# Optimization experiments

Hardware: AMD Instinct MI355X
Metric: run time of the kernel (lower is better)

## Reference

```python
import jax, jax.numpy as jnp
import numpy as np

B, S, D = 2, 2048, 1024
H, DK = 16, 64            # num_heads, d_kv; inner_dim = H*DK = 1024
NUM_BUCKETS = 32
MAX_DISTANCE = 128


def _relative_position_bucket(relative_position, bidirectional=True,
                              num_buckets=NUM_BUCKETS, max_distance=MAX_DISTANCE):
    # Faithful port of Mesh-TF / HF T5 bucketing (int32 in, int32 buckets out).
    relative_buckets = jnp.zeros_like(relative_position)
    if bidirectional:
        num_buckets = num_buckets // 2
        relative_buckets = relative_buckets + (relative_position > 0).astype(jnp.int32) * num_buckets
        relative_position = jnp.abs(relative_position)
    else:
        relative_position = -jnp.minimum(relative_position, 0)
    max_exact = num_buckets // 2
    is_small = relative_position < max_exact
    # log-spaced buckets for large distances; guard log(0) (masked by is_small anyway)
    rel_f = jnp.maximum(relative_position, 1).astype(jnp.float32)
    val_if_large = max_exact + (
        jnp.log(rel_f / max_exact) / np.log(max_distance / max_exact) * (num_buckets - max_exact)
    ).astype(jnp.int32)
    val_if_large = jnp.minimum(val_if_large, num_buckets - 1)
    return relative_buckets + jnp.where(is_small, relative_position, val_if_large)


def compute_bias(rel_emb, query_length, key_length):
    ctx = jnp.arange(query_length, dtype=jnp.int32)[:, None]
    mem = jnp.arange(key_length, dtype=jnp.int32)[None, :]
    buckets = _relative_position_bucket(mem - ctx, bidirectional=True)  # [q, k]
    values = rel_emb[buckets]                       # [q, k, H]
    return jnp.transpose(values, (2, 0, 1))[None]   # [1, H, q, k]


def setup_inputs() -> dict:
    key = jax.random.key(0)
    ks = jax.random.split(key, 6)
    scale = 1.0 / np.sqrt(D)
    return {
        "hidden_states": jax.random.normal(ks[0], (B, S, D), jnp.float32),
        "wq": jax.random.normal(ks[1], (D, H * DK), jnp.float32) * scale,
        "wk": jax.random.normal(ks[2], (D, H * DK), jnp.float32) * scale,
        "wv": jax.random.normal(ks[3], (D, H * DK), jnp.float32) * scale,
        "wo": jax.random.normal(ks[4], (H * DK, D), jnp.float32) * scale,
        "rel_emb": jax.random.normal(ks[5], (NUM_BUCKETS, H), jnp.float32),
    }


def reference(hidden_states, wq, wk, wv, wo, rel_emb):
    b, s, _ = hidden_states.shape

    def shape(x):  # [B,S,H*DK] -> [B,H,S,DK]
        return x.reshape(b, s, H, DK).transpose(0, 2, 1, 3)

    q = shape(hidden_states @ wq)   # NOTE: T5 does not scale q by 1/sqrt(d_kv)
    k = shape(hidden_states @ wk)
    v = shape(hidden_states @ wv)

    scores = jnp.einsum("bhqd,bhkd->bhqk", q, k)
    position_bias = compute_bias(rel_emb, s, s)     # [1,H,S,S]
    scores = scores + position_bias
    attn = jax.nn.softmax(scores, axis=-1)
    ctx = jnp.einsum("bhqk,bhkd->bhqd", attn, v)    # [B,H,S,DK]
    ctx = ctx.transpose(0, 2, 1, 3).reshape(b, s, H * DK)
    return ctx @ wo
```

## Files before the change

kernel.cpp:

```cpp
#include <hip/hip_runtime.h>


typedef __attribute__((ext_vector_type(8)))  unsigned short u16x8;
typedef __attribute__((ext_vector_type(4)))  unsigned short u16x4;
typedef __attribute__((ext_vector_type(8)))  __bf16         bf16x8;
typedef __attribute__((ext_vector_type(4)))  float          f32x4;
typedef __attribute__((ext_vector_type(4)))  unsigned int   u32x4;

#define GLOBAL_AS __attribute__((address_space(1)))
#define LDS_AS    __attribute__((address_space(3)))

static __device__ inline f32x4 MFMA(u16x8 a, u16x8 b, f32x4 c) {
  return __builtin_amdgcn_mfma_f32_16x16x32_bf16(
      __builtin_bit_cast(bf16x8, a), __builtin_bit_cast(bf16x8, b), c, 0, 0, 0);
}

static __device__ inline void gload16(const void* g, void* l) {
  __builtin_amdgcn_global_load_lds((const GLOBAL_AS unsigned int*)g,
                                   (LDS_AS unsigned int*)l, 16, 0, 0);
}

static __device__ inline unsigned short f2bf(float x) {
  unsigned int u = __builtin_bit_cast(unsigned int, x);
  u = (u + 0x7FFFu + ((u >> 16) & 1u)) >> 16;
  return (unsigned short)u;
}

static __device__ inline unsigned int cvtpk(float lo, float hi) {
  unsigned int r;
  asm volatile("v_cvt_pk_bf16_f32 %0, %1, %2" : "=v"(r) : "v"(lo), "v"(hi));
  return r;
}

#define L2E 1.4426950408889634f

__global__ void k_cvt(const float* __restrict__ src, unsigned short* __restrict__ dst, int n4) {
  int i = blockIdx.x * blockDim.x + threadIdx.x;
  if (i >= n4) return;
  float4 v = *(const float4*)(src + (size_t)i * 4);
  u16x4 o;
  o[0] = f2bf(v.x); o[1] = f2bf(v.y); o[2] = f2bf(v.z); o[3] = f2bf(v.w);
  *(u16x4*)(dst + (size_t)i * 4) = o;
}

__global__ __launch_bounds__(256) void k_tc(const float* __restrict__ src,
                                            unsigned short* __restrict__ dst,
                                            int K, int N) {
  __shared__ float tile[64][65];
  int k0 = blockIdx.y << 6, n0 = blockIdx.x << 6;
  int t = threadIdx.x;
  int rr = t >> 4, cc = (t & 15) << 2;
#pragma unroll
  for (int j = 0; j < 4; j++) {
    float4 v = *(const float4*)(src + (size_t)(k0 + rr + j * 16) * N + n0 + cc);
    tile[rr + j * 16][cc + 0] = v.x;
    tile[rr + j * 16][cc + 1] = v.y;
    tile[rr + j * 16][cc + 2] = v.z;
    tile[rr + j * 16][cc + 3] = v.w;
  }
  __syncthreads();
#pragma unroll
  for (int j = 0; j < 4; j++) {
    int n = rr + j * 16;
    u16x4 o;
    o[0] = f2bf(tile[cc + 0][n]);
    o[1] = f2bf(tile[cc + 1][n]);
    o[2] = f2bf(tile[cc + 2][n]);
    o[3] = f2bf(tile[cc + 3][n]);
    *(u16x4*)(dst + (size_t)(n0 + n) * K + k0 + cc) = o;
  }
}

__global__ void k_bias(const float* __restrict__ rel_emb, float* __restrict__ btab) {
  int i = blockIdx.x * blockDim.x + threadIdx.x;
  if (i >= 16 * 4095) return;
  int h = i / 4095;
  int rp = i % 4095 - 2047;
  int rb = rp > 0 ? 16 : 0;
  int arp = rp < 0 ? -rp : rp;
  int v;
  if (arp < 8) {
    v = arp;
  } else {
    float t = logf((float)arp * 0.125f);
    t = t / 2.772588722239781f;
    t = t * 8.0f;
    v = 8 + (int)t;
    if (v > 15) v = 15;
  }
  btab[i] = rel_emb[(rb + v) * 16 + h] * L2E;
}

template <int EPI>
__global__ __launch_bounds__(256) void k_gemm(const unsigned short* __restrict__ A,
                                              const unsigned short* __restrict__ Bt,
                                              void* __restrict__ outp,
                                              int M, int N, int K) {
  __shared__ __attribute__((aligned(16))) char smem[32768];
  const int tid = threadIdx.x;
  const int lane = tid & 63, w = tid >> 6;
  const int l15 = lane & 15, g = lane >> 4;
  const int wr = w >> 1, wc = w & 1;
  const int bm0 = blockIdx.y << 7, bn0 = blockIdx.x << 7;

  const char* Ag = (const char*)A + (size_t)bm0 * K * 2;
  const char* Bg = (const char*)Bt + (size_t)bn0 * K * 2;

  f32x4 acc[4][4];
#pragma unroll
  for (int i = 0; i < 4; i++)
#pragma unroll
    for (int j = 0; j < 4; j++) acc[i][j] = (f32x4)0.0f;

  const int rowA = wr * 64 + l15;
  const int rowB = wc * 64 + l15;
  const int swz = (l15 & 7) << 4;

  for (int kt = 0; kt < K; kt += 64) {
#pragma unroll
    for (int j = 0; j < 4; j++) {
      int idx = ((j * 4 + w) << 10) + (lane << 4);
      int row = idx >> 7;
      int gs = (idx >> 4) & 7;
      size_t co = (size_t)row * (K * 2) + kt * 2 + ((gs ^ (row & 7)) << 4);
      gload16(Ag + co, smem + ((j * 4 + w) << 10));
      gload16(Bg + co, smem + 16384 + ((j * 4 + w) << 10));
    }
    __syncthreads();
#pragma unroll
    for (int kk = 0; kk < 2; kk++) {
      const int cp = ((kk << 6) + (g << 4)) ^ swz;
      u16x8 af[4], bfv[4];
#pragma unroll
      for (int mt = 0; mt < 4; mt++)
        af[mt] = *(const u16x8*)(smem + ((rowA + mt * 16) << 7) + cp);
#pragma unroll
      for (int nt = 0; nt < 4; nt++)
        bfv[nt] = *(const u16x8*)(smem + 16384 + ((rowB + nt * 16) << 7) + cp);
#pragma unroll
      for (int mt = 0; mt < 4; mt++)
#pragma unroll
        for (int nt = 0; nt < 4; nt++)
          acc[mt][nt] = MFMA(af[mt], bfv[nt], acc[mt][nt]);
    }
    __syncthreads();
  }

#pragma unroll
  for (int mt = 0; mt < 4; mt++) {
#pragma unroll
    for (int nt = 0; nt < 4; nt++) {
#pragma unroll
      for (int r = 0; r < 4; r++) {
        int m = bm0 + wr * 64 + mt * 16 + g * 4 + r;
        int n = bn0 + wc * 64 + nt * 16 + l15;
        float val = acc[mt][nt][r];
        if (EPI == 0) {
          int which = n >> 10;
          int hh = (n >> 6) & 15;
          int d = n & 63;
          int bb = m >> 11, s = m & 2047;
          int plane = bb * 16 + hh;
          unsigned short* o = (unsigned short*)outp;
          if (which == 0) {
            o[(size_t)plane * 131072 + (size_t)s * 64 + d] = f2bf(val * L2E);
          } else if (which == 1) {
            o[4194304 + (size_t)plane * 131072 + (size_t)s * 64 + d] = f2bf(val);
          } else {
            o[8388608 + (size_t)plane * 131072 + (size_t)d * 2048 + s] = f2bf(val);
          }
        } else {
          ((float*)outp)[(size_t)m * N + n] = val;
        }
      }
    }
  }
}

__global__ __launch_bounds__(512, 6) void k_attn(const unsigned short* __restrict__ qkv,
                                                 const float* __restrict__ btab,
                                                 unsigned short* __restrict__ ctx) {
  __shared__ __attribute__((aligned(16))) char smem[32768];
  const int tid = threadIdx.x;
  const int lane = tid & 63, w = tid >> 6;
  const int l15 = lane & 15, g = lane >> 4;

  const int wg = ((blockIdx.x & 7) << 6) + (blockIdx.x >> 3);
  const int plane = wg >> 4, qb = wg & 15;
  const int h = plane & 15, b = plane >> 4;
  const int q0 = (qb << 7) + (w << 4);

  const unsigned short* Qp = qkv + (size_t)plane * 131072;
  const unsigned short* Kp = qkv + 4194304 + (size_t)plane * 131072;
  const unsigned short* Vt = qkv + 8388608 + (size_t)plane * 131072;

  u16x8 qa[2];
#pragma unroll
  for (int kk = 0; kk < 2; kk++)
    qa[kk] = *(const u16x8*)(Qp + (size_t)(q0 + l15) * 64 + kk * 32 + g * 8);

  float m_r = -1e30f;
  f32x4 oacc[4], lacc;
#pragma unroll
  for (int t = 0; t < 4; t++) oacc[t] = (f32x4)0.0f;
  lacc = (f32x4)0.0f;

  const float* brow = btab + h * 4095 + 2047 - q0;
  const float cpos = btab[h * 4095 + 2047 + 1024];
  const float cneg = btab[h * 4095 + 2047 - 1024];

  u16x8 ones;
  {
    u32x4 ov = {0x3F803F80u, 0x3F803F80u, 0x3F803F80u, 0x3F803F80u};
    ones = __builtin_bit_cast(u16x8, ov);
  }

  const int srow = (w << 3) + (lane >> 3);
  const int soff = ((lane & 7) ^ (srow & 7)) << 4;
  const char* Ksrc = (const char*)Kp + (size_t)srow * 128 + soff;
  const char* Vsrc = (const char*)Vt + (size_t)srow * 4096 + soff;

  auto STAGE = [&](int t, int bsel) {
    char* sb = smem + (bsel << 14) + (w << 10);
    gload16(Ksrc + (size_t)t * 8192, sb);
    gload16(Vsrc + (size_t)t * 128, sb + 8192);
  };

  STAGE(0, 0);
  __syncthreads();

  for (int t = 0; t < 32; ++t) {
    const int c = t & 1;
    if (t < 31) STAGE(t + 1, c ^ 1);
    const char* kb = smem + (c << 14);
    const char* vbuf = kb + 8192;
    const int kv = t << 6;

    f32x4 s[4];
    __builtin_amdgcn_s_setprio(1);
#pragma unroll
    for (int nt = 0; nt < 4; nt++) {
      int keyr = nt * 16 + l15;
      int sw = (keyr & 7) << 4;
      u16x8 kb0 = *(const u16x8*)(kb + (keyr << 7) + ((g << 4) ^ sw));
      u16x8 kb1 = *(const u16x8*)(kb + (keyr << 7) + ((64 + (g << 4)) ^ sw));
      f32x4 z = (f32x4)0.0f;
      z = MFMA(kb0, qa[0], z);
      z = MFMA(kb1, qa[1], z);
      s[nt] = z;
    }
    __builtin_amdgcn_s_setprio(0);

    int delta = kv - q0;
    float cb;
    if (delta >= 112 || delta <= -160) {
      cb = delta > 0 ? cpos : cneg;
    } else {
      cb = 0.0f;
      const float* bp = brow + kv + (g << 2) - l15;
#pragma unroll
      for (int nt = 0; nt < 4; nt++)
#pragma unroll
        for (int r = 0; r < 4; r++) s[nt][r] += bp[nt * 16 + r];
    }

    float m1 = fmaxf(fmaxf(s[0][0], s[0][1]), s[0][2]);
    float m2 = fmaxf(fmaxf(s[0][3], s[1][0]), s[1][1]);
    float m3 = fmaxf(fmaxf(s[1][2], s[1][3]), s[2][0]);
    float m4 = fmaxf(fmaxf(s[2][1], s[2][2]), s[2][3]);
    float m5 = fmaxf(fmaxf(s[3][0], s[3][1]), s[3][2]);
    float mloc = fmaxf(fmaxf(fmaxf(m1, m2), fmaxf(m3, m4)), fmaxf(m5, s[3][3]));

    if (!__all(mloc + cb <= m_r + 12.0f)) {
      float mxrow = fmaxf(mloc, __shfl_xor(mloc, 16));
      mxrow = fmaxf(mxrow, __shfl_xor(mxrow, 32));
      float mnew = fmaxf(m_r, mxrow + cb);
      float alpha = exp2f(m_r - mnew);
      m_r = mnew;
      float a4[4];
#pragma unroll
      for (int r = 0; r < 4; r++) a4[r] = __shfl(alpha, (g << 2) + r);
#pragma unroll
      for (int tt = 0; tt < 4; tt++) {
        f32x4 o = oacc[tt];
        o[0] *= a4[0]; o[1] *= a4[1]; o[2] *= a4[2]; o[3] *= a4[3];
        oacc[tt] = o;
      }
      lacc[0] *= a4[0]; lacc[1] *= a4[1]; lacc[2] *= a4[2]; lacc[3] *= a4[3];
    }

    float eb = cb - m_r;
#pragma unroll
    for (int nt = 0; nt < 4; nt++)
#pragma unroll
      for (int r = 0; r < 4; r++)
        s[nt][r] = __builtin_amdgcn_exp2f(s[nt][r] + eb);

    unsigned int wpk[4][2];
#pragma unroll
    for (int nt = 0; nt < 4; nt++) {
      wpk[nt][0] = cvtpk(s[nt][0], s[nt][1]);
      wpk[nt][1] = cvtpk(s[nt][2], s[nt][3]);
    }
    u16x8 pa[2];
#pragma unroll
    for (int kk = 0; kk < 2; kk++) {
      unsigned int X0 = wpk[2 * kk][0], Y0 = wpk[2 * kk + 1][0];
      asm volatile("v_permlane32_swap_b32 %0, %1" : "+v"(X0), "+v"(Y0));
      asm volatile("v_permlane16_swap_b32 %0, %1" : "+v"(X0), "+v"(Y0));
      unsigned int X1 = wpk[2 * kk][1], Y1 = wpk[2 * kk + 1][1];
      asm volatile("v_permlane32_swap_b32 %0, %1" : "+v"(X1), "+v"(Y1));
      asm volatile("v_permlane16_swap_b32 %0, %1" : "+v"(X1), "+v"(Y1));
      u32x4 pw = {X0, X1, Y0, Y1};
      pa[kk] = __builtin_bit_cast(u16x8, pw);
    }

    __builtin_amdgcn_s_setprio(1);
#pragma unroll
    for (int tt = 0; tt < 4; tt++) {
      int d = tt * 16 + l15;
      int sw = (d & 7) << 4;
      u16x8 vb0 = *(const u16x8*)(vbuf + (d << 7) + ((g << 4) ^ sw));
      u16x8 vb1 = *(const u16x8*)(vbuf + (d << 7) + ((64 + (g << 4)) ^ sw));
      oacc[tt] = MFMA(pa[0], vb0, oacc[tt]);
      oacc[tt] = MFMA(pa[1], vb1, oacc[tt]);
    }
    lacc = MFMA(pa[0], ones, lacc);
    lacc = MFMA(pa[1], ones, lacc);
    __builtin_amdgcn_s_setprio(0);

    __syncthreads();
  }

#pragma unroll
  for (int r = 0; r < 4; r++) {
    float inv = 1.0f / lacc[r];
    size_t rowoff = ((size_t)(b * 2048 + q0 + (g << 2) + r) << 10) + h * 64;
#pragma unroll
    for (int tt = 0; tt < 4; tt++)
      ctx[rowoff + tt * 16 + l15] = f2bf(oacc[tt][r] * inv);
  }
}

extern "C" void kernel_launch(void* const* d_in, const int* in_sizes, int n_in,
                              void* d_out, int out_size, void* d_ws, size_t ws_size,
                              hipStream_t stream) {
  const float* hs = (const float*)d_in[0];
  const float* wq = (const float*)d_in[1];
  const float* wk = (const float*)d_in[2];
  const float* wv = (const float*)d_in[3];
  const float* wo = (const float*)d_in[4];
  const float* re = (const float*)d_in[5];

  if (ws_size < 50593728u) return;

  char* ws = (char*)d_ws;
  unsigned short* hsb = (unsigned short*)(ws);
  unsigned short* wt  = (unsigned short*)(ws + 8388608);
  unsigned short* wot = (unsigned short*)(ws + 14680064);
  unsigned short* qkv = (unsigned short*)(ws + 16777216);
  unsigned short* ctx = (unsigned short*)(ws + 41943040);
  float*          btab = (float*)(ws + 50331648);

  k_cvt<<<4096, 256, 0, stream>>>(hs, hsb, 1048576);
  k_tc<<<dim3(16, 16), 256, 0, stream>>>(wq, wt, 1024, 1024);
  k_tc<<<dim3(16, 16), 256, 0, stream>>>(wk, wt + 1048576, 1024, 1024);
  k_tc<<<dim3(16, 16), 256, 0, stream>>>(wv, wt + 2097152, 1024, 1024);
  k_tc<<<dim3(16, 16), 256, 0, stream>>>(wo, wot, 1024, 1024);
  k_bias<<<256, 256, 0, stream>>>(re, btab);

  k_gemm<0><<<dim3(24, 32), 256, 0, stream>>>(hsb, wt, qkv, 4096, 3072, 1024);
  k_attn<<<512, 512, 0, stream>>>(qkv, btab, ctx);
  k_gemm<1><<<dim3(8, 32), 256, 0, stream>>>(ctx, wot, d_out, 4096, 1024, 1024);
}
```

Baseline: 134.5 us.

## Fuse prep kernels into one launch and triple-buffer attention K/V staging

```diff
diff --git a/kernel.cpp b/kernel.cpp
--- a/kernel.cpp
+++ b/kernel.cpp
@@ -34,61 +34,76 @@
 
 #define L2E 1.4426950408889634f
 
-__global__ void k_cvt(const float* __restrict__ src, unsigned short* __restrict__ dst, int n4) {
-  int i = blockIdx.x * blockDim.x + threadIdx.x;
-  if (i >= n4) return;
-  float4 v = *(const float4*)(src + (size_t)i * 4);
-  u16x4 o;
-  o[0] = f2bf(v.x); o[1] = f2bf(v.y); o[2] = f2bf(v.z); o[3] = f2bf(v.w);
-  *(u16x4*)(dst + (size_t)i * 4) = o;
-}
-
-__global__ __launch_bounds__(256) void k_tc(const float* __restrict__ src,
-                                            unsigned short* __restrict__ dst,
-                                            int K, int N) {
+__global__ __launch_bounds__(256) void k_prep(const float* __restrict__ hs,
+                                              const float* __restrict__ wq,
+                                              const float* __restrict__ wk,
+                                              const float* __restrict__ wv,
+                                              const float* __restrict__ wo,
+                                              const float* __restrict__ re,
+                                              unsigned short* __restrict__ hsb,
+                                              unsigned short* __restrict__ wt,
+                                              unsigned short* __restrict__ wot,
+                                              float* __restrict__ btab) {
   __shared__ float tile[64][65];
-  int k0 = blockIdx.y << 6, n0 = blockIdx.x << 6;
-  int t = threadIdx.x;
-  int rr = t >> 4, cc = (t & 15) << 2;
-#pragma unroll
-  for (int j = 0; j < 4; j++) {
-    float4 v = *(const float4*)(src + (size_t)(k0 + rr + j * 16) * N + n0 + cc);
-    tile[rr + j * 16][cc + 0] = v.x;
-    tile[rr + j * 16][cc + 1] = v.y;
-    tile[rr + j * 16][cc + 2] = v.z;
-    tile[rr + j * 16][cc + 3] = v.w;
-  }
-  __syncthreads();
-#pragma unroll
-  for (int j = 0; j < 4; j++) {
-    int n = rr + j * 16;
+  const int bid = blockIdx.x;
+  const int t = threadIdx.x;
+
+  if (bid < 4096) {
+    int i = bid * 256 + t;
+    float4 v = *(const float4*)(hs + (size_t)i * 4);
     u16x4 o;
-    o[0] = f2bf(tile[cc + 0][n]);
-    o[1] = f2bf(tile[cc + 1][n]);
-    o[2] = f2bf(tile[cc + 2][n]);
-    o[3] = f2bf(tile[cc + 3][n]);
-    *(u16x4*)(dst + (size_t)(n0 + n) * K + k0 + cc) = o;
-  }
-}
-
-__global__ void k_bias(const float* __restrict__ rel_emb, float* __restrict__ btab) {
-  int i = blockIdx.x * blockDim.x + threadIdx.x;
-  if (i >= 16 * 4095) return;
-  int h = i / 4095;
-  int rp = i % 4095 - 2047;
-  int rb = rp > 0 ? 16 : 0;
-  int arp = rp < 0 ? -rp : rp;
-  int v;
-  if (arp < 8) {
-    v = arp;
+    o[0] = f2bf(v.x); o[1] = f2bf(v.y); o[2] = f2bf(v.z); o[3] = f2bf(v.w);
+    *(u16x4*)(hsb + (size_t)i * 4) = o;
+  } else if (bid < 5120) {
+    int sub = bid - 4096;
+    int which = sub >> 8;
+    int sb = sub & 255;
+    int n0 = (sb & 15) << 6, k0 = (sb >> 4) << 6;
+    const float* src = which == 0 ? wq : which == 1 ? wk : which == 2 ? wv : wo;
+    unsigned short* dst = which == 0 ? wt
+                        : which == 1 ? wt + 1048576
+                        : which == 2 ? wt + 2097152 : wot;
+    const int K = 1024, N = 1024;
+    int rr = t >> 4, cc = (t & 15) << 2;
+#pragma unroll
+    for (int j = 0; j < 4; j++) {
+      float4 v = *(const float4*)(src + (size_t)(k0 + rr + j * 16) * N + n0 + cc);
+      tile[rr + j * 16][cc + 0] = v.x;
+      tile[rr + j * 16][cc + 1] = v.y;
+      tile[rr + j * 16][cc + 2] = v.z;
+      tile[rr + j * 16][cc + 3] = v.w;
+    }
+    __syncthreads();
+#pragma unroll
+    for (int j = 0; j < 4; j++) {
+      int n = rr + j * 16;
+      u16x4 o;
+      o[0] = f2bf(tile[cc + 0][n]);
+      o[1] = f2bf(tile[cc + 1][n]);
+      o[2] = f2bf(tile[cc + 2][n]);
+      o[3] = f2bf(tile[cc + 3][n]);
+      *(u16x4*)(dst + (size_t)(n0 + n) * K + k0 + cc) = o;
+    }
   } else {
-    float t = logf((float)arp * 0.125f);
-    t = t / 2.772588722239781f;
-    t = t * 8.0f;
-    v = 8 + (int)t;
-    if (v > 15) v = 15;
-  }
-  btab[i] = rel_emb[(rb + v) * 16 + h] * L2E;
+    int i = (bid - 5120) * 256 + t;
+    if (i < 16 * 4095) {
+      int h = i / 4095;
+      int rp = i % 4095 - 2047;
+      int rb = rp > 0 ? 16 : 0;
+      int arp = rp < 0 ? -rp : rp;
+      int v;
+      if (arp < 8) {
+        v = arp;
+      } else {
+        float tt = logf((float)arp * 0.125f);
+        tt = tt / 2.772588722239781f;
+        tt = tt * 8.0f;
+        v = 8 + (int)tt;
+        if (v > 15) v = 15;
+      }
+      btab[i] = re[(rb + v) * 16 + h] * L2E;
+    }
+  }
 }
 
 template <int EPI>
@@ -180,7 +195,7 @@
 __global__ __launch_bounds__(512, 6) void k_attn(const unsigned short* __restrict__ qkv,
                                                  const float* __restrict__ btab,
                                                  unsigned short* __restrict__ ctx) {
-  __shared__ __attribute__((aligned(16))) char smem[32768];
+  __shared__ __attribute__((aligned(16))) char smem[49152];
   const int tid = threadIdx.x;
   const int lane = tid & 63, w = tid >> 6;
   const int l15 = lane & 15, g = lane >> 4;
@@ -221,19 +236,25 @@
   const char* Vsrc = (const char*)Vt + (size_t)srow * 4096 + soff;
 
   auto STAGE = [&](int t, int bsel) {
-    char* sb = smem + (bsel << 14) + (w << 10);
+    char* sb = smem + bsel * 16384 + (w << 10);
     gload16(Ksrc + (size_t)t * 8192, sb);
     gload16(Vsrc + (size_t)t * 128, sb + 8192);
   };
 
   STAGE(0, 0);
-  __syncthreads();
-
+  STAGE(1, 1);
+
+  int rb = 0, sbn = 2;
   for (int t = 0; t < 32; ++t) {
-    const int c = t & 1;
-    if (t < 31) STAGE(t + 1, c ^ 1);
-    const char* kb = smem + (c << 14);
+    if (t < 30) { asm volatile("s_waitcnt vmcnt(2)" ::: "memory"); }
+    else        { asm volatile("s_waitcnt vmcnt(0)" ::: "memory"); }
+    asm volatile("s_waitcnt lgkmcnt(0)" ::: "memory");
+    __builtin_amdgcn_s_barrier();
+    __builtin_amdgcn_sched_barrier(0);
+    if (t < 30) { STAGE(t + 2, sbn); sbn = (sbn == 2) ? 0 : sbn + 1; }
+    const char* kb = smem + rb * 16384;
     const char* vbuf = kb + 8192;
+    rb = (rb == 2) ? 0 : rb + 1;
     const int kv = t << 6;
 
     f32x4 s[4];
@@ -328,8 +349,6 @@
     lacc = MFMA(pa[0], ones, lacc);
     lacc = MFMA(pa[1], ones, lacc);
     __builtin_amdgcn_s_setprio(0);
-
-    __syncthreads();
   }
 
 #pragma unroll
@@ -362,13 +381,7 @@
   unsigned short* ctx = (unsigned short*)(ws + 41943040);
   float*          btab = (float*)(ws + 50331648);
 
-  k_cvt<<<4096, 256, 0, stream>>>(hs, hsb, 1048576);
-  k_tc<<<dim3(16, 16), 256, 0, stream>>>(wq, wt, 1024, 1024);
-  k_tc<<<dim3(16, 16), 256, 0, stream>>>(wk, wt + 1048576, 1024, 1024);
-  k_tc<<<dim3(16, 16), 256, 0, stream>>>(wv, wt + 2097152, 1024, 1024);
-  k_tc<<<dim3(16, 16), 256, 0, stream>>>(wo, wot, 1024, 1024);
-  k_bias<<<256, 256, 0, stream>>>(re, btab);
-
+  k_prep<<<5376, 256, 0, stream>>>(hs, wq, wk, wv, wo, re, hsb, wt, wot, btab);
   k_gemm<0><<<dim3(24, 32), 256, 0, stream>>>(hsb, wt, qkv, 4096, 3072, 1024);
   k_attn<<<512, 512, 0, stream>>>(qkv, btab, ctx);
   k_gemm<1><<<dim3(8, 32), 256, 0, stream>>>(ctx, wot, d_out, 4096, 1024, 1024);
```

Result: faster. 126.3 us (-6.1%).
